# Performance work log

Hardware: AMD Instinct MI355X
Metric: run time of the kernel (lower is better)

Reference implementation:

```python
import jax, jax.numpy as jnp
import numpy as np

KERNEL_SIZES = [1, 2, 3]
KERNEL_NUM = 11
SIGMA = 0.1
EXACT_SIGMA = 0.001
EMBED_DIM = 300
HIDDEN = 128
Q_VOCAB = 30000
D_VOCAB = 30000


def _mus_sigmas():
    mus, sigmas = [], []
    K = KERNEL_NUM
    for i in range(K):
        mu = 1.0 / (K - 1) + 2.0 * i / (K - 1) - 1.0
        sigma = SIGMA
        if mu > 1.0:
            sigma = EXACT_SIGMA
            mu = 1.0
        mus.append(mu)
        sigmas.append(sigma)
    return jnp.asarray(mus, jnp.float32), jnp.asarray(sigmas, jnp.float32)


def _conv_tanh(x_bcl, w, b, ks):
    # x_bcl: (B, C_in, L); ConstantPad1d((0, ks)) + Conv1d(kernel=ks+1) keeps length L
    y = jax.lax.conv_general_dilated(
        x_bcl, w, window_strides=(1,), padding=[(0, ks)],
        dimension_numbers=('NCW', 'OIW', 'NCW'))
    return jnp.tanh(y + b[None, :, None])  # (B, H, L)


def _l2norm(x):
    n = jnp.sqrt(jnp.sum(x * x, axis=-1, keepdims=True))
    return x / jnp.maximum(n, 1e-12)


def setup_inputs() -> dict:
    key = jax.random.key(0)
    ks = jax.random.split(key, 16)
    inp = {
        'query': jax.random.randint(ks[0], (128, 128), 0, Q_VOCAB),
        'doc': jax.random.randint(ks[1], (128, 512), 0, D_VOCAB),
        'q_emb': jax.random.normal(ks[2], (Q_VOCAB, EMBED_DIM), jnp.float32) * 0.1,
        'd_emb': jax.random.normal(ks[3], (D_VOCAB, EMBED_DIM), jnp.float32) * 0.1,
        'out_w': jax.random.normal(ks[4], (1, 3 * 3 * KERNEL_NUM), jnp.float32) * 0.1,
        'out_b': jnp.zeros((1,), jnp.float32),
    }
    for idx, k in enumerate(KERNEL_SIZES):
        fan_in = EMBED_DIM * (k + 1)
        inp[f'conv_w{idx}'] = jax.random.normal(ks[5 + 2 * idx], (HIDDEN, EMBED_DIM, k + 1), jnp.float32) / np.sqrt(fan_in)
        inp[f'conv_b{idx}'] = jnp.zeros((HIDDEN,), jnp.float32)
    return inp


def reference(query, doc, q_emb, d_emb, conv_w0, conv_b0, conv_w1, conv_b1,
              conv_w2, conv_b2, out_w, out_b):
    mus, sigmas = _mus_sigmas()
    inv2s2 = 1.0 / (2.0 * sigmas * sigmas)  # (K,)

    q_e = q_emb[query].transpose(0, 2, 1)  # (B, D, Lq)
    d_e = d_emb[doc].transpose(0, 2, 1)    # (B, D, Ld)

    cws = [(conv_w0, conv_b0), (conv_w1, conv_b1), (conv_w2, conv_b2)]
    # q_convs/d_convs share weights (same nn.Sequential appended to both lists)
    q_convs = [_l2norm(_conv_tanh(q_e, w, b, ks).transpose(0, 2, 1))
               for (w, b), ks in zip(cws, KERNEL_SIZES)]  # each (B, Lq, H)
    d_convs = [_l2norm(_conv_tanh(d_e, w, b, ks).transpose(0, 2, 1))
               for (w, b), ks in zip(cws, KERNEL_SIZES)]  # each (B, Ld, H)

    KM = []
    for qi in range(3):
        for di in range(3):
            mm = jnp.einsum('bld,brd->blr', q_convs[qi], d_convs[di])  # (B,Lq,Ld)
            # Gaussian kernel soft-histogram, vectorized over all kernels
            kern = jnp.exp(-(mm[..., None] - mus) ** 2 * inv2s2)  # (B,Lq,Ld,K)
            K = jnp.log1p(kern.sum(axis=2)).sum(axis=1)           # (B,K)
            KM.append(K)
    phi = jnp.concatenate(KM, axis=1)  # (B, 9*KERNEL_NUM)
    return phi @ out_w.T + out_b       # (B, 1)
```

## Files before the change

### kernel.cpp

```cpp
#include <hip/hip_runtime.h>
#include <hip/hip_bf16.h>

typedef __hip_bfloat16 bf16;
typedef __attribute__((ext_vector_type(8))) short short8;
typedef __attribute__((ext_vector_type(4))) float f32x4;
typedef __attribute__((ext_vector_type(2))) float f32x2;

#define NB 128
#define NH 128
#define NLQ 128
#define NLD 512
#define NEMB 300
#define XQROWS 132
#define XDROWS 516
#define XCOLS 320

__device__ __forceinline__ unsigned short bfbits(float x) {
    __hip_bfloat16 h = __float2bfloat16(x);
    return *reinterpret_cast<unsigned short*>(&h);
}

__device__ __forceinline__ float fast_tanh(float x) {
    x = fminf(9.f, fmaxf(-9.f, x));
    float e = __builtin_amdgcn_exp2f(x * 2.8853900817779268f);
    return (e - 1.f) * __builtin_amdgcn_rcpf(e + 1.f);
}

__global__ __launch_bounds__(256)
void pack_all(const int* __restrict__ q_tok, const int* __restrict__ d_tok,
              const float* __restrict__ q_emb, const float* __restrict__ d_emb,
              const float* __restrict__ cw0, const float* __restrict__ cw1,
              const float* __restrict__ cw2,
              bf16* __restrict__ Wp, bf16* __restrict__ Xq, bf16* __restrict__ Xd)
{
    int bx = blockIdx.x;
    if (bx < 1440) {
        int e = bx * 256 + threadIdx.x;
        int widx = (e >= 204800) ? 2 : (e >= 81920 ? 1 : 0);
        int off = (widx == 0) ? 0 : (widx == 1 ? 81920 : 204800);
        int el = e - off;
        int W = widx + 2;
        int ch = el >> 12;
        int cc = ch / W;
        int t  = ch - cc * W;
        int h  = (el >> 5) & 127;
        int cp = el & 31;
        int c  = cc * 32 + cp;
        const float* cw = (widx == 0) ? cw0 : (widx == 1 ? cw1 : cw2);
        float v = (c < NEMB) ? cw[(h * NEMB + c) * W + t] : 0.f;
        Wp[e] = __float2bfloat16(v);
        return;
    }
    int gid = (bx - 1440) * 256 + threadIdx.x;
    int row = gid / 20, g = gid - row * 20;
    const float* emb; bf16* dst; int tok;
    if (row < NB * XQROWS) {
        int b = row / XQROWS, l = row - b * XQROWS;
        tok = (l < NLQ) ? q_tok[b * NLQ + l] : -1;
        emb = q_emb;
        dst = Xq + (size_t)row * XCOLS + g * 16;
    } else {
        int rowd = row - NB * XQROWS;
        int b = rowd / XDROWS, l = rowd - b * XDROWS;
        tok = (l < NLD) ? d_tok[b * NLD + l] : -1;
        emb = d_emb;
        dst = Xd + (size_t)rowd * XCOLS + g * 16;
    }
    int c0 = g * 16;
    float4 v[4];
    #pragma unroll
    for (int q = 0; q < 4; ++q) {
        int c = c0 + q * 4;
        v[q] = make_float4(0.f, 0.f, 0.f, 0.f);
        if (tok >= 0 && c < NEMB)
            v[q] = *reinterpret_cast<const float4*>(emb + (size_t)tok * NEMB + c);
    }
    short8 o0, o1;
    o0[0] = (short)bfbits(v[0].x); o0[1] = (short)bfbits(v[0].y);
    o0[2] = (short)bfbits(v[0].z); o0[3] = (short)bfbits(v[0].w);
    o0[4] = (short)bfbits(v[1].x); o0[5] = (short)bfbits(v[1].y);
    o0[6] = (short)bfbits(v[1].z); o0[7] = (short)bfbits(v[1].w);
    o1[0] = (short)bfbits(v[2].x); o1[1] = (short)bfbits(v[2].y);
    o1[2] = (short)bfbits(v[2].z); o1[3] = (short)bfbits(v[2].w);
    o1[4] = (short)bfbits(v[3].x); o1[5] = (short)bfbits(v[3].y);
    o1[6] = (short)bfbits(v[3].z); o1[7] = (short)bfbits(v[3].w);
    *reinterpret_cast<short8*>(dst) = o0;
    *reinterpret_cast<short8*>(dst + 8) = o1;
}

__global__ __launch_bounds__(512, 4)
void conv_kernel(const bf16* __restrict__ Xq, const bf16* __restrict__ Xd,
                 const bf16* __restrict__ Wp,
                 const float* __restrict__ cb0, const float* __restrict__ cb1,
                 const float* __restrict__ cb2,
                 bf16* __restrict__ qn, bf16* __restrict__ dn)
{
    __shared__ bf16 Xs[2][2][132][40];
    __shared__ float ssq[2][256];

    int bx = blockIdx.x;
    int widx = bx % 3;
    int inner = bx / 3;
    int W = widx + 2;
    const bf16* wp = Wp + ((widx == 0) ? 0 : (widx == 1 ? 81920 : 204800));
    const float* cb = (widx == 0) ? cb0 : (widx == 1 ? cb1 : cb2);

    int tid = threadIdx.x;
    int lane = tid & 63;
    int wv = tid >> 6;
    int wr = wv >> 1;
    int wc = wv & 1;
    int s_wave = wr >> 1;
    int lr_base = (wr & 1) * 64;

    bf16* outp; int L;
    int sb0, sb1, sl00, sl01;
    const bf16* xbase;
    size_t grow0, grow1;
    if (inner < 64) {
        outp = qn + (size_t)widx * NB * NLQ * NH;
        L = NLQ; sb0 = inner * 2; sb1 = sb0 + 1; sl00 = 0; sl01 = 0;
        xbase = Xq; grow0 = (size_t)sb0 * XQROWS; grow1 = (size_t)sb1 * XQROWS;
    } else {
        int i = inner - 64;
        outp = dn + (size_t)widx * NB * NLD * NH;
        L = NLD; sb0 = i >> 1; sb1 = sb0; sl00 = (i & 1) * 256; sl01 = sl00 + 128;
        xbase = Xd; grow0 = (size_t)sb0 * XDROWS + sl00; grow1 = grow0 + 128;
    }

    int sr = tid >> 2;
    int colg = tid & 3;
    const bf16* gsrc0 = xbase + (grow0 + sr) * XCOLS + colg * 8;
    const bf16* gsrc1 = xbase + (grow1 + sr) * XCOLS + colg * 8;
    bool has_tail = (tid >= 448 && tid < 480);
    int j = tid - 448;
    int ts = (j >> 2) >> 2, trr = 128 + ((j >> 2) & 3), tcolg = j & 3;
    const bf16* gsrcT = xbase + ((ts ? grow1 : grow0) + trr) * XCOLS + tcolg * 8;

    short8 a0, a1, at;
    a0 = *reinterpret_cast<const short8*>(gsrc0);
    a1 = *reinterpret_cast<const short8*>(gsrc1);
    if (has_tail) at = *reinterpret_cast<const short8*>(gsrcT);
    *reinterpret_cast<short8*>(&Xs[0][0][sr][colg * 8]) = a0;
    *reinterpret_cast<short8*>(&Xs[0][1][sr][colg * 8]) = a1;
    if (has_tail) *reinterpret_cast<short8*>(&Xs[0][ts][trr][tcolg * 8]) = at;
    __syncthreads();

    f32x4 acc[4][4];
    #pragma unroll
    for (int m = 0; m < 4; ++m)
        #pragma unroll
        for (int n = 0; n < 4; ++n)
            acc[m][n] = (f32x4){0.f, 0.f, 0.f, 0.f};

    const bf16* pB = wp + ((size_t)((wc * 64 + (lane & 15)) * 4 + (lane >> 4))) * 8;

    int cur = 0, step = 0;
    for (int cc = 0; cc < 10; ++cc) {
        if (cc < 9) {
            a0 = *reinterpret_cast<const short8*>(gsrc0 + (cc + 1) * 32);
            a1 = *reinterpret_cast<const short8*>(gsrc1 + (cc + 1) * 32);
            if (has_tail) at = *reinterpret_cast<const short8*>(gsrcT + (cc + 1) * 32);
        }
        for (int t = 0; t < W; ++t, ++step) {
            const bf16* pBs = pB + (size_t)step * 4096;
            short8 bv[4], af[4];
            #pragma unroll
            for (int n = 0; n < 4; ++n)
                bv[n] = *reinterpret_cast<const short8*>(pBs + n * 512);
            #pragma unroll
            for (int m = 0; m < 4; ++m)
                af[m] = *reinterpret_cast<const short8*>(
                    &Xs[cur][s_wave][lr_base + m * 16 + (lane & 15) + t][(lane >> 4) * 8]);
            #pragma unroll
            for (int m = 0; m < 4; ++m)
                #pragma unroll
                for (int n = 0; n < 4; ++n)
                    acc[m][n] = __builtin_amdgcn_mfma_f32_16x16x32_bf16(af[m], bv[n], acc[m][n], 0, 0, 0);
        }
        if (cc < 9) {
            *reinterpret_cast<short8*>(&Xs[cur ^ 1][0][sr][colg * 8]) = a0;
            *reinterpret_cast<short8*>(&Xs[cur ^ 1][1][sr][colg * 8]) = a1;
            if (has_tail) *reinterpret_cast<short8*>(&Xs[cur ^ 1][ts][trr][tcolg * 8]) = at;
            __syncthreads();
            cur ^= 1;
        }
    }

    float ssl[4][4];
    #pragma unroll
    for (int m = 0; m < 4; ++m)
        #pragma unroll
        for (int i = 0; i < 4; ++i) ssl[m][i] = 0.f;

    #pragma unroll
    for (int n = 0; n < 4; ++n) {
        float bias = cb[wc * 64 + n * 16 + (lane & 15)];
        #pragma unroll
        for (int m = 0; m < 4; ++m)
            #pragma unroll
            for (int i = 0; i < 4; ++i) {
                float v = fast_tanh(acc[m][n][i] + bias);
                acc[m][n][i] = v;
                ssl[m][i] += v * v;
            }
    }
    #pragma unroll
    for (int m = 0; m < 4; ++m)
        #pragma unroll
        for (int i = 0; i < 4; ++i) {
            float s = ssl[m][i];
            s += __shfl_xor(s, 1); s += __shfl_xor(s, 2);
            s += __shfl_xor(s, 4); s += __shfl_xor(s, 8);
            ssl[m][i] = s;
        }
    if ((lane & 15) == 0) {
        #pragma unroll
        for (int m = 0; m < 4; ++m)
            #pragma unroll
            for (int i = 0; i < 4; ++i)
                ssq[wc][wr * 64 + m * 16 + (lane >> 4) * 4 + i] = ssl[m][i];
    }
    __syncthreads();
    #pragma unroll
    for (int m = 0; m < 4; ++m)
        #pragma unroll
        for (int i = 0; i < 4; ++i) {
            int r = wr * 64 + m * 16 + (lane >> 4) * 4 + i;
            float s2 = ssq[0][r] + ssq[1][r];
            float sc = 1.f / fmaxf(sqrtf(s2), 1e-12f);
            int s = r >> 7, lr = r & 127;
            int b = s ? sb1 : sb0;
            int l = (s ? sl01 : sl00) + lr;
            bf16* dst = outp + ((size_t)(b * L + l)) * NH;
            #pragma unroll
            for (int n = 0; n < 4; ++n)
                dst[wc * 64 + n * 16 + (lane & 15)] = __float2bfloat16(acc[m][n][i] * sc);
        }
}

__global__ __launch_bounds__(512, 4)
void sim_kernel(const bf16* __restrict__ qn, const bf16* __restrict__ dn,
                float* __restrict__ phi)
{
    __shared__ bf16 Qs[128][136];
    __shared__ bf16 Ds[64][136];
    __shared__ float wsum[2][11];
    float (*red)[128][11] = reinterpret_cast<float(*)[128][11]>(&Ds[0][0]);

    int blk = blockIdx.x;
    int b = blk / 9;
    int pair = blk - b * 9;
    int qi = pair / 3, di = pair - qi * 3;

    int tid = threadIdx.x, lane = tid & 63, wv = tid >> 6;
    int wr = wv >> 2;
    int wc = wv & 3;

    const bf16* qbase = qn + ((size_t)qi * NB + b) * (NLQ * NH);
    const bf16* dbase = dn + ((size_t)di * NB + b) * (NLD * NH);

    {
        int r = tid >> 2, h0 = (tid & 3) * 32;
        #pragma unroll
        for (int v = 0; v < 4; ++v)
            *reinterpret_cast<short8*>(&Qs[r][h0 + v * 8]) =
                *reinterpret_cast<const short8*>(qbase + (size_t)r * NH + h0 + v * 8);
    }

    int dr = tid >> 3, dc = (tid & 7) * 16;
    {
        short8 st[2];
        #pragma unroll
        for (int v = 0; v < 2; ++v)
            st[v] = *reinterpret_cast<const short8*>(dbase + (size_t)dr * NH + dc + v * 8);
        #pragma unroll
        for (int v = 0; v < 2; ++v)
            *reinterpret_cast<short8*>(&Ds[dr][dc + v * 8]) = st[v];
    }
    __syncthreads();

    f32x2 sums2[2][11];
    #pragma unroll
    for (int n = 0; n < 2; ++n)
        #pragma unroll
        for (int k = 0; k < 11; ++k) sums2[n][k] = (f32x2){0.f, 0.f};

    const float C1 = 1.8315638888734179e-2f;
    const float C2 = 3.3546262790251185e-4f;
    const float C3 = 6.1442123533282098e-6f;
    const float C4 = 1.1253517471925912e-7f;

    for (int cc = 0; cc < 8; ++cc) {
        f32x4 acc[2][2];
        #pragma unroll
        for (int m = 0; m < 2; ++m)
            #pragma unroll
            for (int n = 0; n < 2; ++n)
                acc[m][n] = (f32x4){0.f, 0.f, 0.f, 0.f};

        #pragma unroll
        for (int kc = 0; kc < 4; ++kc) {
            short8 af[2], bq[2];
            #pragma unroll
            for (int m = 0; m < 2; ++m)
                af[m] = *reinterpret_cast<const short8*>(
                    &Ds[wr * 32 + m * 16 + (lane & 15)][kc * 32 + (lane >> 4) * 8]);
            #pragma unroll
            for (int n = 0; n < 2; ++n)
                bq[n] = *reinterpret_cast<const short8*>(
                    &Qs[wc * 32 + n * 16 + (lane & 15)][kc * 32 + (lane >> 4) * 8]);
            #pragma unroll
            for (int m = 0; m < 2; ++m)
                #pragma unroll
                for (int n = 0; n < 2; ++n)
                    acc[m][n] = __builtin_amdgcn_mfma_f32_16x16x32_bf16(af[m], bq[n], acc[m][n], 0, 0, 0);
        }
        __syncthreads();

        short8 st[2];
        if (cc < 7) {
            #pragma unroll
            for (int v = 0; v < 2; ++v)
                st[v] = *reinterpret_cast<const short8*>(
                    dbase + (size_t)((cc + 1) * 64 + dr) * NH + dc + v * 8);
        }

        #pragma unroll
        for (int n = 0; n < 2; ++n)
            #pragma unroll
            for (int i = 0; i < 4; ++i) {
                f32x2 x2;
                x2.x = acc[0][n][i];
                x2.y = acc[1][n][i];
                f32x2 ax = x2 * 28.853900817779268f;
                f32x2 R, Ri, E4;
                R.x = __builtin_amdgcn_exp2f(ax.x);
                R.y = __builtin_amdgcn_exp2f(ax.y);
                Ri.x = __builtin_amdgcn_rcpf(R.x);
                Ri.y = __builtin_amdgcn_rcpf(R.y);
                f32x2 d4 = x2 + 0.1f;
                f32x2 t = d4 * d4 * (-72.134752044448169f);
                E4.x = __builtin_amdgcn_exp2f(t.x);
                E4.y = __builtin_amdgcn_exp2f(t.y);
                sums2[n][4] += E4;
                f32x2 u = E4 * R;
                sums2[n][5] += u;
                u *= R; u *= C1; sums2[n][6] += u;
                u *= R; u *= C2; sums2[n][7] += u;
                u *= R; u *= C3; sums2[n][8] += u;
                u *= R; u *= C4; sums2[n][9] += u;
                f32x2 w = E4 * Ri; w *= C1; sums2[n][3] += w;
                w *= Ri; w *= C2; sums2[n][2] += w;
                w *= Ri; w *= C3; sums2[n][1] += w;
                w *= Ri; w *= C4; sums2[n][0] += w;
                if (__any(fmaxf(x2.x, x2.y) > 0.98f)) {
                    f32x2 d1 = x2 - 1.0f;
                    f32x2 t1 = d1 * d1 * (-721347.52044448f);
                    f32x2 e;
                    e.x = __builtin_amdgcn_exp2f(t1.x);
                    e.y = __builtin_amdgcn_exp2f(t1.y);
                    sums2[n][10] += e;
                }
            }

        if (cc < 7) {
            #pragma unroll
            for (int v = 0; v < 2; ++v)
                *reinterpret_cast<short8*>(&Ds[dr][dc + v * 8]) = st[v];
            __syncthreads();
        }
    }

    #pragma unroll
    for (int n = 0; n < 2; ++n)
        #pragma unroll
        for (int k = 0; k < 11; ++k) {
            float s = sums2[n][k].x + sums2[n][k].y;
            s += __shfl_xor(s, 16);
            s += __shfl_xor(s, 32);
            sums2[n][k].x = s;
        }
    if ((lane >> 4) == 0) {
        #pragma unroll
        for (int n = 0; n < 2; ++n)
            #pragma unroll
            for (int k = 0; k < 11; ++k)
                red[wr][wc * 32 + n * 16 + (lane & 15)][k] = sums2[n][k].x;
    }
    __syncthreads();
    if (tid < 128) {
        float lv[11];
        #pragma unroll
        for (int k = 0; k < 11; ++k)
            lv[k] = log1pf(red[0][tid][k] + red[1][tid][k]);
        #pragma unroll
        for (int k = 0; k < 11; ++k) {
            float s = lv[k];
            s += __shfl_xor(s, 1); s += __shfl_xor(s, 2); s += __shfl_xor(s, 4);
            s += __shfl_xor(s, 8); s += __shfl_xor(s, 16); s += __shfl_xor(s, 32);
            lv[k] = s;
        }
        if ((tid & 63) == 0) {
            #pragma unroll
            for (int k = 0; k < 11; ++k) wsum[tid >> 6][k] = lv[k];
        }
    }
    __syncthreads();
    if (tid < 11) phi[b * 99 + pair * 11 + tid] = wsum[0][tid] + wsum[1][tid];
}

__global__ void final_kernel(const float* __restrict__ phi, const float* __restrict__ ow,
                             const float* __restrict__ obias, float* __restrict__ out)
{
    int b = threadIdx.x;
    float s = obias[0];
    #pragma unroll
    for (int j = 0; j < 99; ++j) s += phi[b * 99 + j] * ow[j];
    out[b] = s;
}

extern "C" void kernel_launch(void* const* d_in, const int* in_sizes, int n_in,
                              void* d_out, int out_size, void* d_ws, size_t ws_size,
                              hipStream_t stream)
{
    const int*   query = (const int*)d_in[0];
    const int*   doc   = (const int*)d_in[1];
    const float* q_emb = (const float*)d_in[2];
    const float* d_emb = (const float*)d_in[3];
    const float* out_w = (const float*)d_in[4];
    const float* out_b = (const float*)d_in[5];
    const float* cw0 = (const float*)d_in[6];
    const float* cb0 = (const float*)d_in[7];
    const float* cw1 = (const float*)d_in[8];
    const float* cb1 = (const float*)d_in[9];
    const float* cw2 = (const float*)d_in[10];
    const float* cb2 = (const float*)d_in[11];

    const size_t QN = (size_t)NB * NLQ * NH;
    const size_t DN = (size_t)NB * NLD * NH;
    const size_t XQN = (size_t)NB * XQROWS * XCOLS;
    const size_t XDN = (size_t)NB * XDROWS * XCOLS;

    bf16* Wp = (bf16*)d_ws;
    bf16* Xq = Wp + 368640;
    bf16* Xd = Xq + XQN;
    bf16* qn = Xd + XDN;
    bf16* dn = qn + 3 * QN;
    float* phi = (float*)(dn + 3 * DN);

    pack_all<<<7920, 256, 0, stream>>>(query, doc, q_emb, d_emb, cw0, cw1, cw2, Wp, Xq, Xd);
    conv_kernel<<<960, 512, 0, stream>>>(Xq, Xd, Wp, cb0, cb1, cb2, qn, dn);
    sim_kernel<<<NB * 9, 512, 0, stream>>>(qn, dn, phi);
    final_kernel<<<1, 128, 0, stream>>>(phi, out_w, out_b, (float*)d_out);
}
```

Baseline: 219.6 us.

## Restructure conv kernel so one block computes all three filter widths per tile

Each conv block now loads a 64-row token tile with the full 320-column embedding into shared memory once, and its six waves compute all three convolution widths (two column halves per width). Before, each block handled a single width over two 128-row tiles and streamed 32-column chunks through a double buffer. The change is meant to stop reading the same embedding rows three times and to drop the per-chunk barriers. In exchange it uses more LDS per block, has no overlap between global loads and MFMA work, and gives waves uneven work because wider filters take more steps.

```diff
diff --git a/kernel.cpp b/kernel.cpp
--- a/kernel.cpp
+++ b/kernel.cpp
@@ -88,63 +88,53 @@
     *reinterpret_cast<short8*>(dst + 8) = o1;
 }
 
-__global__ __launch_bounds__(512, 4)
+__global__ __launch_bounds__(384, 3)
 void conv_kernel(const bf16* __restrict__ Xq, const bf16* __restrict__ Xd,
                  const bf16* __restrict__ Wp,
                  const float* __restrict__ cb0, const float* __restrict__ cb1,
                  const float* __restrict__ cb2,
                  bf16* __restrict__ qn, bf16* __restrict__ dn)
 {
-    __shared__ bf16 Xs[2][2][132][40];
-    __shared__ float ssq[2][256];
-
-    int bx = blockIdx.x;
-    int widx = bx % 3;
-    int inner = bx / 3;
-    int W = widx + 2;
-    const bf16* wp = Wp + ((widx == 0) ? 0 : (widx == 1 ? 81920 : 204800));
-    const float* cb = (widx == 0) ? cb0 : (widx == 1 ? cb1 : cb2);
-
+    __shared__ bf16 Xs[68][328];
+    __shared__ float ssq[6][64];
+
+    const size_t QN = (size_t)NB * NLQ * NH;
+    const size_t DN = (size_t)NB * NLD * NH;
+
+    int inner = blockIdx.x;
     int tid = threadIdx.x;
     int lane = tid & 63;
     int wv = tid >> 6;
-    int wr = wv >> 1;
-    int wc = wv & 1;
-    int s_wave = wr >> 1;
-    int lr_base = (wr & 1) * 64;
-
-    bf16* outp; int L;
-    int sb0, sb1, sl00, sl01;
-    const bf16* xbase;
-    size_t grow0, grow1;
-    if (inner < 64) {
-        outp = qn + (size_t)widx * NB * NLQ * NH;
-        L = NLQ; sb0 = inner * 2; sb1 = sb0 + 1; sl00 = 0; sl01 = 0;
-        xbase = Xq; grow0 = (size_t)sb0 * XQROWS; grow1 = (size_t)sb1 * XQROWS;
+    int widx_w = wv >> 1;
+    int Ww = widx_w + 2;
+    int colh = wv & 1;
+
+    bool is_q = (inner < 256);
+    const bf16* xbase; size_t grow; int b, l0, L;
+    if (is_q) {
+        b = inner >> 1; l0 = (inner & 1) * 64; L = NLQ;
+        xbase = Xq; grow = (size_t)b * XQROWS + l0;
     } else {
-        int i = inner - 64;
-        outp = dn + (size_t)widx * NB * NLD * NH;
-        L = NLD; sb0 = i >> 1; sb1 = sb0; sl00 = (i & 1) * 256; sl01 = sl00 + 128;
-        xbase = Xd; grow0 = (size_t)sb0 * XDROWS + sl00; grow1 = grow0 + 128;
-    }
-
-    int sr = tid >> 2;
-    int colg = tid & 3;
-    const bf16* gsrc0 = xbase + (grow0 + sr) * XCOLS + colg * 8;
-    const bf16* gsrc1 = xbase + (grow1 + sr) * XCOLS + colg * 8;
-    bool has_tail = (tid >= 448 && tid < 480);
-    int j = tid - 448;
-    int ts = (j >> 2) >> 2, trr = 128 + ((j >> 2) & 3), tcolg = j & 3;
-    const bf16* gsrcT = xbase + ((ts ? grow1 : grow0) + trr) * XCOLS + tcolg * 8;
-
-    short8 a0, a1, at;
-    a0 = *reinterpret_cast<const short8*>(gsrc0);
-    a1 = *reinterpret_cast<const short8*>(gsrc1);
-    if (has_tail) at = *reinterpret_cast<const short8*>(gsrcT);
-    *reinterpret_cast<short8*>(&Xs[0][0][sr][colg * 8]) = a0;
-    *reinterpret_cast<short8*>(&Xs[0][1][sr][colg * 8]) = a1;
-    if (has_tail) *reinterpret_cast<short8*>(&Xs[0][ts][trr][tcolg * 8]) = at;
+        int i = inner - 256;
+        b = i >> 3; l0 = (i & 7) * 64; L = NLD;
+        xbase = Xd; grow = (size_t)b * XDROWS + l0;
+    }
+
+    for (int u = tid; u < 68 * 20; u += 384) {
+        int row = u / 20, cg = u - row * 20;
+        const short8* src = reinterpret_cast<const short8*>(
+            xbase + (grow + row) * XCOLS + cg * 16);
+        short8 s0 = src[0], s1 = src[1];
+        *reinterpret_cast<short8*>(&Xs[row][cg * 16]) = s0;
+        *reinterpret_cast<short8*>(&Xs[row][cg * 16 + 8]) = s1;
+    }
     __syncthreads();
+
+    const bf16* wp = Wp + ((widx_w == 0) ? 0 : (widx_w == 1 ? 81920 : 204800));
+    const float* cb_w = (widx_w == 0) ? cb0 : (widx_w == 1 ? cb1 : cb2);
+    bf16* outp = (is_q ? qn + (size_t)widx_w * QN : dn + (size_t)widx_w * DN);
+
+    const bf16* pB = wp + ((size_t)((colh * 64 + (lane & 15)) * 4 + (lane >> 4))) * 8;
 
     f32x4 acc[4][4];
     #pragma unroll
@@ -153,16 +143,9 @@
         for (int n = 0; n < 4; ++n)
             acc[m][n] = (f32x4){0.f, 0.f, 0.f, 0.f};
 
-    const bf16* pB = wp + ((size_t)((wc * 64 + (lane & 15)) * 4 + (lane >> 4))) * 8;
-
-    int cur = 0, step = 0;
+    int step = 0;
     for (int cc = 0; cc < 10; ++cc) {
-        if (cc < 9) {
-            a0 = *reinterpret_cast<const short8*>(gsrc0 + (cc + 1) * 32);
-            a1 = *reinterpret_cast<const short8*>(gsrc1 + (cc + 1) * 32);
-            if (has_tail) at = *reinterpret_cast<const short8*>(gsrcT + (cc + 1) * 32);
-        }
-        for (int t = 0; t < W; ++t, ++step) {
+        for (int t = 0; t < Ww; ++t, ++step) {
             const bf16* pBs = pB + (size_t)step * 4096;
             short8 bv[4], af[4];
             #pragma unroll
@@ -171,20 +154,13 @@
             #pragma unroll
             for (int m = 0; m < 4; ++m)
                 af[m] = *reinterpret_cast<const short8*>(
-                    &Xs[cur][s_wave][lr_base + m * 16 + (lane & 15) + t][(lane >> 4) * 8]);
+                    &Xs[m * 16 + (lane & 15) + t][cc * 32 + (lane >> 4) * 8]);
             #pragma unroll
             for (int m = 0; m < 4; ++m)
                 #pragma unroll
                 for (int n = 0; n < 4; ++n)
                     acc[m][n] = __builtin_amdgcn_mfma_f32_16x16x32_bf16(af[m], bv[n], acc[m][n], 0, 0, 0);
         }
-        if (cc < 9) {
-            *reinterpret_cast<short8*>(&Xs[cur ^ 1][0][sr][colg * 8]) = a0;
-            *reinterpret_cast<short8*>(&Xs[cur ^ 1][1][sr][colg * 8]) = a1;
-            if (has_tail) *reinterpret_cast<short8*>(&Xs[cur ^ 1][ts][trr][tcolg * 8]) = at;
-            __syncthreads();
-            cur ^= 1;
-        }
     }
 
     float ssl[4][4];
@@ -195,7 +171,7 @@
 
     #pragma unroll
     for (int n = 0; n < 4; ++n) {
-        float bias = cb[wc * 64 + n * 16 + (lane & 15)];
+        float bias = cb_w[colh * 64 + n * 16 + (lane & 15)];
         #pragma unroll
         for (int m = 0; m < 4; ++m)
             #pragma unroll
@@ -219,23 +195,21 @@
         for (int m = 0; m < 4; ++m)
             #pragma unroll
             for (int i = 0; i < 4; ++i)
-                ssq[wc][wr * 64 + m * 16 + (lane >> 4) * 4 + i] = ssl[m][i];
+                ssq[wv][m * 16 + (lane >> 4) * 4 + i] = ssl[m][i];
     }
     __syncthreads();
+    int wpair = widx_w << 1;
     #pragma unroll
     for (int m = 0; m < 4; ++m)
         #pragma unroll
         for (int i = 0; i < 4; ++i) {
-            int r = wr * 64 + m * 16 + (lane >> 4) * 4 + i;
-            float s2 = ssq[0][r] + ssq[1][r];
+            int r = m * 16 + (lane >> 4) * 4 + i;
+            float s2 = ssq[wpair][r] + ssq[wpair + 1][r];
             float sc = 1.f / fmaxf(sqrtf(s2), 1e-12f);
-            int s = r >> 7, lr = r & 127;
-            int b = s ? sb1 : sb0;
-            int l = (s ? sl01 : sl00) + lr;
-            bf16* dst = outp + ((size_t)(b * L + l)) * NH;
+            bf16* dst = outp + ((size_t)(b * L + l0 + r)) * NH;
             #pragma unroll
             for (int n = 0; n < 4; ++n)
-                dst[wc * 64 + n * 16 + (lane & 15)] = __float2bfloat16(acc[m][n][i] * sc);
+                dst[colh * 64 + n * 16 + (lane & 15)] = __float2bfloat16(acc[m][n][i] * sc);
         }
 }
 
@@ -450,7 +424,7 @@
     float* phi = (float*)(dn + 3 * DN);
 
     pack_all<<<7920, 256, 0, stream>>>(query, doc, q_emb, d_emb, cw0, cw1, cw2, Wp, Xq, Xd);
-    conv_kernel<<<960, 512, 0, stream>>>(Xq, Xd, Wp, cb0, cb1, cb2, qn, dn);
+    conv_kernel<<<1280, 384, 0, stream>>>(Xq, Xd, Wp, cb0, cb1, cb2, qn, dn);
     sim_kernel<<<NB * 9, 512, 0, stream>>>(qn, dn, phi);
     final_kernel<<<1, 128, 0, stream>>>(phi, out_w, out_b, (float*)d_out);
 }
```

Result: no change. 221.9 us (+1.1%).

## Stage conv weight tiles through double-buffered shared memory

Applied to the files above, without the earlier changes.

Conv weight fragments are no longer read directly from global memory by every wave. Each step's 128x32 weight tile is now loaded cooperatively into a double-buffered LDS array, prefetched one step ahead, and all waves read their B fragments from LDS. This removes redundant global loads of the same weights by the four row-waves. In exchange it adds a __syncthreads per inner step, extra LDS traffic and more LDS footprint, which may reduce occupancy.

```diff
diff --git a/kernel.cpp b/kernel.cpp
--- a/kernel.cpp
+++ b/kernel.cpp
@@ -96,6 +96,7 @@
                  bf16* __restrict__ qn, bf16* __restrict__ dn)
 {
     __shared__ bf16 Xs[2][2][132][40];
+    __shared__ bf16 Bs[2][128][36];
     __shared__ float ssq[2][256];
 
     int bx = blockIdx.x;
@@ -137,13 +138,20 @@
     int ts = (j >> 2) >> 2, trr = 128 + ((j >> 2) & 3), tcolg = j & 3;
     const bf16* gsrcT = xbase + ((ts ? grow1 : grow0) + trr) * XCOLS + tcolg * 8;
 
-    short8 a0, a1, at;
-    a0 = *reinterpret_cast<const short8*>(gsrc0);
-    a1 = *reinterpret_cast<const short8*>(gsrc1);
-    if (has_tail) at = *reinterpret_cast<const short8*>(gsrcT);
-    *reinterpret_cast<short8*>(&Xs[0][0][sr][colg * 8]) = a0;
-    *reinterpret_cast<short8*>(&Xs[0][1][sr][colg * 8]) = a1;
-    if (has_tail) *reinterpret_cast<short8*>(&Xs[0][ts][trr][tcolg * 8]) = at;
+    const short8* wp8 = reinterpret_cast<const short8*>(wp);
+    int bh = tid >> 2, bcg = tid & 3;
+
+    {
+        short8 a0 = *reinterpret_cast<const short8*>(gsrc0);
+        short8 a1 = *reinterpret_cast<const short8*>(gsrc1);
+        short8 at;
+        if (has_tail) at = *reinterpret_cast<const short8*>(gsrcT);
+        short8 b0 = wp8[tid];
+        *reinterpret_cast<short8*>(&Xs[0][0][sr][colg * 8]) = a0;
+        *reinterpret_cast<short8*>(&Xs[0][1][sr][colg * 8]) = a1;
+        if (has_tail) *reinterpret_cast<short8*>(&Xs[0][ts][trr][tcolg * 8]) = at;
+        *reinterpret_cast<short8*>(&Bs[0][bh][bcg * 8]) = b0;
+    }
     __syncthreads();
 
     f32x4 acc[4][4];
@@ -153,9 +161,9 @@
         for (int n = 0; n < 4; ++n)
             acc[m][n] = (f32x4){0.f, 0.f, 0.f, 0.f};
 
-    const bf16* pB = wp + ((size_t)((wc * 64 + (lane & 15)) * 4 + (lane >> 4))) * 8;
-
-    int cur = 0, step = 0;
+    int nsteps = W * 10;
+    int xcur = 0, bcur = 0, step = 0;
+    short8 a0, a1, at;
     for (int cc = 0; cc < 10; ++cc) {
         if (cc < 9) {
             a0 = *reinterpret_cast<const short8*>(gsrc0 + (cc + 1) * 32);
@@ -163,27 +171,35 @@
             if (has_tail) at = *reinterpret_cast<const short8*>(gsrcT + (cc + 1) * 32);
         }
         for (int t = 0; t < W; ++t, ++step) {
-            const bf16* pBs = pB + (size_t)step * 4096;
+            short8 nb;
+            bool hn = (step + 1 < nsteps);
+            if (hn) nb = wp8[(size_t)(step + 1) * 512 + tid];
+
             short8 bv[4], af[4];
             #pragma unroll
             for (int n = 0; n < 4; ++n)
-                bv[n] = *reinterpret_cast<const short8*>(pBs + n * 512);
+                bv[n] = *reinterpret_cast<const short8*>(
+                    &Bs[bcur][wc * 64 + n * 16 + (lane & 15)][(lane >> 4) * 8]);
             #pragma unroll
             for (int m = 0; m < 4; ++m)
                 af[m] = *reinterpret_cast<const short8*>(
-                    &Xs[cur][s_wave][lr_base + m * 16 + (lane & 15) + t][(lane >> 4) * 8]);
+                    &Xs[xcur][s_wave][lr_base + m * 16 + (lane & 15) + t][(lane >> 4) * 8]);
             #pragma unroll
             for (int m = 0; m < 4; ++m)
                 #pragma unroll
                 for (int n = 0; n < 4; ++n)
                     acc[m][n] = __builtin_amdgcn_mfma_f32_16x16x32_bf16(af[m], bv[n], acc[m][n], 0, 0, 0);
-        }
-        if (cc < 9) {
-            *reinterpret_cast<short8*>(&Xs[cur ^ 1][0][sr][colg * 8]) = a0;
-            *reinterpret_cast<short8*>(&Xs[cur ^ 1][1][sr][colg * 8]) = a1;
-            if (has_tail) *reinterpret_cast<short8*>(&Xs[cur ^ 1][ts][trr][tcolg * 8]) = at;
-            __syncthreads();
-            cur ^= 1;
+
+            if (hn)
+                *reinterpret_cast<short8*>(&Bs[bcur ^ 1][bh][bcg * 8]) = nb;
+            if (t == W - 1 && cc < 9) {
+                *reinterpret_cast<short8*>(&Xs[xcur ^ 1][0][sr][colg * 8]) = a0;
+                *reinterpret_cast<short8*>(&Xs[xcur ^ 1][1][sr][colg * 8]) = a1;
+                if (has_tail) *reinterpret_cast<short8*>(&Xs[xcur ^ 1][ts][trr][tcolg * 8]) = at;
+            }
+            if (hn || (t == W - 1 && cc < 9)) __syncthreads();
+            bcur ^= 1;
+            if (t == W - 1) xcur ^= 1;
         }
     }
 
```

Result: faster. 209.4 us (-4.6%).
